# Kernel optimization log

Hardware: AMD Instinct MI355X
Metric: run time of the kernel (lower is better)

The kernel has to match this reference:

```python
import jax, jax.numpy as jnp
import numpy as np

N, E = 50000, 800000
DIN, DH, DOUT = 128, 128, 64


def setup_inputs() -> dict:
    key = jax.random.key(0)
    ks = jax.random.split(key, 18)
    s = 0.05
    inp = {
        "x": jax.random.normal(ks[0], (N, DIN), dtype=jnp.float32),
        "edge_index": jax.random.randint(ks[1], (2, E), 0, N, dtype=jnp.int64),
        # conv1 MLP: Linear(DIN,DH), Linear(DH,DH)
        "c1_w1": jax.random.normal(ks[2], (DIN, DH), dtype=jnp.float32) * s,
        "c1_b1": jax.random.normal(ks[3], (DH,), dtype=jnp.float32) * s,
        "c1_w2": jax.random.normal(ks[4], (DH, DH), dtype=jnp.float32) * s,
        "c1_b2": jax.random.normal(ks[5], (DH,), dtype=jnp.float32) * s,
        # conv2 MLP
        "c2_w1": jax.random.normal(ks[6], (DH, DH), dtype=jnp.float32) * s,
        "c2_b1": jax.random.normal(ks[7], (DH,), dtype=jnp.float32) * s,
        "c2_w2": jax.random.normal(ks[8], (DH, DH), dtype=jnp.float32) * s,
        "c2_b2": jax.random.normal(ks[9], (DH,), dtype=jnp.float32) * s,
        # conv3 MLP
        "c3_w1": jax.random.normal(ks[10], (DH, DH), dtype=jnp.float32) * s,
        "c3_b1": jax.random.normal(ks[11], (DH,), dtype=jnp.float32) * s,
        "c3_w2": jax.random.normal(ks[12], (DH, DH), dtype=jnp.float32) * s,
        "c3_b2": jax.random.normal(ks[13], (DH,), dtype=jnp.float32) * s,
        # output head
        "lin1_w": jax.random.normal(ks[14], (DH, DH), dtype=jnp.float32) * s,
        "lin1_b": jax.random.normal(ks[15], (DH,), dtype=jnp.float32) * s,
        "lin2_w": jax.random.normal(ks[16], (DH, DOUT), dtype=jnp.float32) * s,
        "lin2_b": jax.random.normal(ks[17], (DOUT,), dtype=jnp.float32) * s,
    }
    return inp


def _gin_conv(h, src, dst, w1, b1, w2, b2):
    # PyG GINConv, eps=0: MLP((1+eps)*x + sum_{j->i} x_j)
    agg = jax.ops.segment_sum(h[src], dst, num_segments=h.shape[0])  # [N, D]
    z = h + agg
    z = jax.nn.relu(z @ w1 + b1)
    return jax.nn.relu(z @ w2 + b2)


def reference(x, edge_index, c1_w1, c1_b1, c1_w2, c1_b2,
              c2_w1, c2_b1, c2_w2, c2_b2,
              c3_w1, c3_b1, c3_w2, c3_b2,
              lin1_w, lin1_b, lin2_w, lin2_b):
    src, dst = edge_index[0], edge_index[1]
    h = _gin_conv(x, src, dst, c1_w1, c1_b1, c1_w2, c1_b2)
    h = jax.nn.relu(h)  # redundant after MLP ReLU, but faithful to source
    h = _gin_conv(h, src, dst, c2_w1, c2_b1, c2_w2, c2_b2)
    h = jax.nn.relu(h)
    h = _gin_conv(h, src, dst, c3_w1, c3_b1, c3_w2, c3_b2)
    h = jax.nn.relu(h @ lin1_w + lin1_b)
    return h @ lin2_w + lin2_b  # [N, DOUT]
```

## Files before the change

### kernel.cpp

```cpp
#include <hip/hip_runtime.h>
#include <hip/hip_bf16.h>

typedef __attribute__((ext_vector_type(8))) short bf16x8;
typedef __attribute__((ext_vector_type(4))) float f32x4;

#define DH 128
#define DOUT 64

static __device__ __forceinline__ unsigned short f2bf(float f) {
    __hip_bfloat16 h = __float2bfloat16(f);
    return *(unsigned short*)&h;
}
static __device__ __forceinline__ void acc2(float& a0, float& a1, unsigned int u) {
    a0 += __uint_as_float(u << 16);
    a1 += __uint_as_float(u & 0xffff0000u);
}


struct WPrep {
    const float* src[8];
    unsigned short* dst[8];
};

__global__ void prep_kernel(const float* __restrict__ x, unsigned short* __restrict__ xb,
                            int n4, WPrep p, int* __restrict__ cnt, int N_) {
    int id = blockIdx.x * blockDim.x + threadIdx.x;
    if (id < n4) {
        float4 v = ((const float4*)x)[id];
        ushort4 b;
        b.x = f2bf(v.x); b.y = f2bf(v.y); b.z = f2bf(v.z); b.w = f2bf(v.w);
        ((ushort4*)xb)[id] = b;
        return;
    }
    id -= n4;
    if (id < N_) { cnt[id] = 0; return; }
    id -= N_;
    int m, off;
    if (id < 7 * 16384) { m = id >> 14; off = id & 16383; }
    else {
        m = 7; off = id - 7 * 16384;
        if (off >= 8192) return;
    }
    int shift = (m == 7) ? 6 : 7;
    int nc = 1 << shift;
    int k = off >> shift;
    int n = off & (nc - 1);
    p.dst[m][n * 128 + k] = f2bf(p.src[m][off]);
}


__global__ void hist_kernel(const int* __restrict__ dst, int* __restrict__ cnt,
                            int* __restrict__ rank, int E, int n) {
    int e = blockIdx.x * blockDim.x + threadIdx.x;
    if (e < E) {
        int d = dst[e];
        if ((unsigned)d < (unsigned)n) rank[e] = atomicAdd(&cnt[d], 1);
    }
}

__global__ void scan1_kernel(const int* __restrict__ cnt, int* __restrict__ rp_part,
                             int* __restrict__ bsum, int n) {
    __shared__ int s[256];
    int tid = threadIdx.x;
    int i = blockIdx.x * 256 + tid;
    int v = (i < n) ? cnt[i] : 0;
    s[tid] = v;
    __syncthreads();
    for (int off = 1; off < 256; off <<= 1) {
        int t = (tid >= off) ? s[tid - off] : 0;
        __syncthreads();
        s[tid] += t;
        __syncthreads();
    }
    if (i < n) rp_part[i] = s[tid] - v;
    if (tid == 255) bsum[blockIdx.x] = s[255];
}

__global__ void scan2_kernel(int* __restrict__ bsum, int nb) {
    __shared__ int s[256];
    int tid = threadIdx.x;
    int v = (tid < nb) ? bsum[tid] : 0;
    s[tid] = v;
    __syncthreads();
    for (int off = 1; off < 256; off <<= 1) {
        int t = (tid >= off) ? s[tid - off] : 0;
        __syncthreads();
        s[tid] += t;
        __syncthreads();
    }
    if (tid < nb) bsum[tid] = s[tid] - v;
}

__global__ void scan3_fill_kernel(const int* __restrict__ rp_part, const int* __restrict__ bsum,
                                  int* __restrict__ row_ptr,
                                  const int* __restrict__ src, const int* __restrict__ dst,
                                  const int* __restrict__ rank, int* __restrict__ esrc,
                                  int n, int E) {
    int gid = blockIdx.x * blockDim.x + threadIdx.x;
    if (gid < n) row_ptr[gid] = rp_part[gid] + bsum[gid >> 8];
    else if (gid == n) row_ptr[n] = E;
    if (gid < E) {
        int d = dst[gid];
        if ((unsigned)d < (unsigned)n)
            esrc[rp_part[d] + bsum[d >> 8] + rank[gid]] = src[gid];
    }
}


template <bool HEAD>
__launch_bounds__(256, 6)
__global__ void layer_kernel(const unsigned short* __restrict__ h,
                             const int* __restrict__ row_ptr,
                             const int* __restrict__ esrc,
                             const unsigned short* __restrict__ W1t,
                             const float* __restrict__ b1,
                             const unsigned short* __restrict__ W2t,
                             const float* __restrict__ b2,
                             const unsigned short* __restrict__ W3t,
                             const float* __restrict__ b3,
                             const unsigned short* __restrict__ W4t,
                             const float* __restrict__ b4,
                             void* __restrict__ outp, int M) {
    constexpr int LDA = 128 + 8;
    __shared__ __align__(16) unsigned short As[16][LDA];
    __shared__ __align__(16) unsigned short Zs[16][LDA];

    int tid = threadIdx.x;
    int wave = __builtin_amdgcn_readfirstlane(tid >> 6);
    int lane = tid & 63;
    int grp = lane >> 4;
    int c = lane & 15;
    int row0 = blockIdx.x * 16;
    int nodes0 = row0 + wave * 4;

    int b[4], e[4];
#pragma unroll
    for (int i = 0; i < 4; ++i) {
        int nd = nodes0 + i;
        b[i] = (nd < M) ? row_ptr[nd] : 0;
        e[i] = (nd < M) ? row_ptr[nd + 1] : 0;
    }
    float acc[4][8];
#pragma unroll
    for (int i = 0; i < 4; ++i)
#pragma unroll
        for (int j = 0; j < 8; ++j) acc[i][j] = 0.f;

    int pos[4];
#pragma unroll
    for (int i = 0; i < 4; ++i) pos[i] = b[i] + grp;
    int itmax = 0;
#pragma unroll
    for (int i = 0; i < 4; ++i) {
        int it = (e[i] - b[i] + 3) >> 2;
        itmax = it > itmax ? it : itmax;
    }

    for (int it = 0; it < itmax; ++it) {
        int idx[4] = {0, 0, 0, 0};
#pragma unroll
        for (int i = 0; i < 4; ++i)
            if (pos[i] < e[i]) idx[i] = esrc[pos[i]];
        uint4 u[4];
#pragma unroll
        for (int i = 0; i < 4; ++i) u[i] = make_uint4(0u, 0u, 0u, 0u);
#pragma unroll
        for (int i = 0; i < 4; ++i)
            if (pos[i] < e[i])
                u[i] = *((const uint4*)((const char*)h + ((size_t)idx[i] << 8)) + c);
#pragma unroll
        for (int i = 0; i < 4; ++i) {
            acc2(acc[i][0], acc[i][1], u[i].x);
            acc2(acc[i][2], acc[i][3], u[i].y);
            acc2(acc[i][4], acc[i][5], u[i].z);
            acc2(acc[i][6], acc[i][7], u[i].w);
            pos[i] += 4;
        }
    }

#pragma unroll
    for (int i = 0; i < 4; ++i) {
        int nd = nodes0 + i;
#pragma unroll
        for (int j = 0; j < 8; ++j) {
            float v = acc[i][j];
            v += __shfl_xor(v, 16, 64);
            v += __shfl_xor(v, 32, 64);
            acc[i][j] = v;
        }
        if (nd < M) {
            uint4 s = *((const uint4*)((const char*)h + ((size_t)nd << 8)) + c);
            acc2(acc[i][0], acc[i][1], s.x);
            acc2(acc[i][2], acc[i][3], s.y);
            acc2(acc[i][4], acc[i][5], s.z);
            acc2(acc[i][6], acc[i][7], s.w);
        }
        if (grp == 0) {
            uint4 ov;
            ov.x = (unsigned)f2bf(acc[i][0]) | ((unsigned)f2bf(acc[i][1]) << 16);
            ov.y = (unsigned)f2bf(acc[i][2]) | ((unsigned)f2bf(acc[i][3]) << 16);
            ov.z = (unsigned)f2bf(acc[i][4]) | ((unsigned)f2bf(acc[i][5]) << 16);
            ov.w = (unsigned)f2bf(acc[i][6]) | ((unsigned)f2bf(acc[i][7]) << 16);
            *(uint4*)(&As[wave * 4 + i][c * 8]) = ov;
        }
    }
    __syncthreads();

    int quad = lane >> 4;
    int l16 = lane & 15;

    bf16x8 af[4];
#pragma unroll
    for (int kt = 0; kt < 4; ++kt)
        af[kt] = *(const bf16x8*)(&As[l16][kt * 32 + quad * 8]);
#pragma unroll
    for (int p = 0; p < 2; ++p) {
        int ncol = (wave * 2 + p) * 16 + l16;
        const unsigned short* wp = W1t + ncol * 128 + quad * 8;
        f32x4 a = {0.f, 0.f, 0.f, 0.f};
#pragma unroll
        for (int kt = 0; kt < 4; ++kt)
            a = __builtin_amdgcn_mfma_f32_16x16x32_bf16(
                af[kt], *(const bf16x8*)(wp + kt * 32), a, 0, 0, 0);
        float bs = b1[ncol];
#pragma unroll
        for (int r = 0; r < 4; ++r) {
            float v = a[r] + bs;
            if (v < 0.f) v = 0.f;
            Zs[quad * 4 + r][ncol] = f2bf(v);
        }
    }
    __syncthreads();

    bf16x8 zf[4];
#pragma unroll
    for (int kt = 0; kt < 4; ++kt)
        zf[kt] = *(const bf16x8*)(&Zs[l16][kt * 32 + quad * 8]);
#pragma unroll
    for (int p = 0; p < 2; ++p) {
        int ncol = (wave * 2 + p) * 16 + l16;
        const unsigned short* wp = W2t + ncol * 128 + quad * 8;
        f32x4 a = {0.f, 0.f, 0.f, 0.f};
#pragma unroll
        for (int kt = 0; kt < 4; ++kt)
            a = __builtin_amdgcn_mfma_f32_16x16x32_bf16(
                zf[kt], *(const bf16x8*)(wp + kt * 32), a, 0, 0, 0);
        float bs = b2[ncol];
#pragma unroll
        for (int r = 0; r < 4; ++r) {
            float v = a[r] + bs;
            if (v < 0.f) v = 0.f;
            if (HEAD) {
                As[quad * 4 + r][ncol] = f2bf(v);
            } else {
                int grow = row0 + quad * 4 + r;
                if (grow < M)
                    ((unsigned short*)outp)[(size_t)grow * 128 + ncol] = f2bf(v);
            }
        }
    }

    if (HEAD) {
        __syncthreads();
        bf16x8 hf[4];
#pragma unroll
        for (int kt = 0; kt < 4; ++kt)
            hf[kt] = *(const bf16x8*)(&As[l16][kt * 32 + quad * 8]);
#pragma unroll
        for (int p = 0; p < 2; ++p) {
            int ncol = (wave * 2 + p) * 16 + l16;
            const unsigned short* wp = W3t + ncol * 128 + quad * 8;
            f32x4 a = {0.f, 0.f, 0.f, 0.f};
#pragma unroll
            for (int kt = 0; kt < 4; ++kt)
                a = __builtin_amdgcn_mfma_f32_16x16x32_bf16(
                    hf[kt], *(const bf16x8*)(wp + kt * 32), a, 0, 0, 0);
            float bs = b3[ncol];
#pragma unroll
            for (int r = 0; r < 4; ++r) {
                float v = a[r] + bs;
                if (v < 0.f) v = 0.f;
                Zs[quad * 4 + r][ncol] = f2bf(v);
            }
        }
        __syncthreads();
        bf16x8 gf[4];
#pragma unroll
        for (int kt = 0; kt < 4; ++kt)
            gf[kt] = *(const bf16x8*)(&Zs[l16][kt * 32 + quad * 8]);
        {
            int ncol = wave * 16 + l16;
            const unsigned short* wp = W4t + ncol * 128 + quad * 8;
            f32x4 a = {0.f, 0.f, 0.f, 0.f};
#pragma unroll
            for (int kt = 0; kt < 4; ++kt)
                a = __builtin_amdgcn_mfma_f32_16x16x32_bf16(
                    gf[kt], *(const bf16x8*)(wp + kt * 32), a, 0, 0, 0);
            float bs = b4[ncol];
#pragma unroll
            for (int r = 0; r < 4; ++r) {
                int grow = row0 + quad * 4 + r;
                if (grow < M)
                    ((float*)outp)[(size_t)grow * 64 + ncol] = a[r] + bs;
            }
        }
    }
}


extern "C" void kernel_launch(void* const* d_in, const int* in_sizes, int n_in,
                              void* d_out, int out_size, void* d_ws, size_t ws_size,
                              hipStream_t stream) {
    const float* x = (const float*)d_in[0];
    const int* ei = (const int*)d_in[1];
    int N = in_sizes[0] / DH;
    int E = in_sizes[1] / 2;
    const int* src = ei;
    const int* dstv = ei + E;

    char* ws = (char*)d_ws;
    size_t off = 0;
    auto alloc = [&](size_t bytes) -> void* {
        void* p = ws + off;
        off += (bytes + 255) & ~(size_t)255;
        return p;
    };
    unsigned short* xb = (unsigned short*)alloc((size_t)N * DH * 2);
    unsigned short* hA = (unsigned short*)alloc((size_t)N * DH * 2);
    unsigned short* hB = (unsigned short*)alloc((size_t)N * DH * 2);
    unsigned short* wt[8];
    for (int m = 0; m < 8; ++m) wt[m] = (unsigned short*)alloc(16384 * 2);
    int* cnt     = (int*)alloc((size_t)N * 4);
    int* rp_part = (int*)alloc((size_t)N * 4);
    int* row_ptr = (int*)alloc((size_t)(N + 1) * 4);
    int* rank    = (int*)alloc((size_t)E * 4);
    int* bsum    = (int*)alloc(256 * 4);
    int* esrc    = (int*)alloc((size_t)E * 4);

    WPrep wp;
    wp.src[0] = (const float*)d_in[2];
    wp.src[1] = (const float*)d_in[4];
    wp.src[2] = (const float*)d_in[6];
    wp.src[3] = (const float*)d_in[8];
    wp.src[4] = (const float*)d_in[10];
    wp.src[5] = (const float*)d_in[12];
    wp.src[6] = (const float*)d_in[14];
    wp.src[7] = (const float*)d_in[16];
    for (int m = 0; m < 8; ++m) wp.dst[m] = wt[m];
    int n4 = N * DH / 4;
    int prep_items = n4 + N + 7 * 16384 + 8192;
    prep_kernel<<<(prep_items + 255) / 256, 256, 0, stream>>>(x, xb, n4, wp, cnt, N);

    int nb = (N + 255) / 256;
    int eb = (E + 255) / 256;
    hist_kernel<<<eb, 256, 0, stream>>>(dstv, cnt, rank, E, N);
    scan1_kernel<<<nb, 256, 0, stream>>>(cnt, rp_part, bsum, N);
    scan2_kernel<<<1, 256, 0, stream>>>(bsum, nb);
    scan3_fill_kernel<<<eb, 256, 0, stream>>>(rp_part, bsum, row_ptr,
                                              src, dstv, rank, esrc, N, E);

    int gb = (N + 15) / 16;

    const float* c1b1 = (const float*)d_in[3];
    const float* c1b2 = (const float*)d_in[5];
    const float* c2b1 = (const float*)d_in[7];
    const float* c2b2 = (const float*)d_in[9];
    const float* c3b1 = (const float*)d_in[11];
    const float* c3b2 = (const float*)d_in[13];
    const float* l1b  = (const float*)d_in[15];
    const float* l2b  = (const float*)d_in[17];

    layer_kernel<false><<<gb, 256, 0, stream>>>(
        xb, row_ptr, esrc, wt[0], c1b1, wt[1], c1b2,
        nullptr, nullptr, nullptr, nullptr, hA, N);
    layer_kernel<false><<<gb, 256, 0, stream>>>(
        hA, row_ptr, esrc, wt[2], c2b1, wt[3], c2b2,
        nullptr, nullptr, nullptr, nullptr, hB, N);
    layer_kernel<true><<<gb, 256, 0, stream>>>(
        hB, row_ptr, esrc, wt[4], c3b1, wt[5], c3b2,
        wt[6], l1b, wt[7], l2b, d_out, N);
}
```

Measured before the change: 364.2 us.

## Pad CSR rows to multiples of 16 with a zero dummy node for branchless gathers

Each node's neighbour count is rounded up to a multiple of 16 in the scan. The padded slots of the edge list point at an extra all-zero row N appended to each feature buffer. The aggregation loop then drops per-edge bounds checks and issues 8 independent row gathers per half-iteration. The self-feature load moves to the start, and launch bounds drop from 6 to 4 blocks per unit to leave room for more registers. The cost is extra gathers of the cached dummy row, a larger esrc buffer that the prep kernel must fill, and unguarded reads if N is not a multiple of 16.

```diff
diff --git a/kernel.cpp b/kernel.cpp
--- a/kernel.cpp
+++ b/kernel.cpp
@@ -14,6 +14,12 @@
 static __device__ __forceinline__ void acc2(float& a0, float& a1, unsigned int u) {
     a0 += __uint_as_float(u << 16);
     a1 += __uint_as_float(u & 0xffff0000u);
+}
+static __device__ __forceinline__ void accq(float* a, const uint4& u) {
+    acc2(a[0], a[1], u.x);
+    acc2(a[2], a[3], u.y);
+    acc2(a[4], a[5], u.z);
+    acc2(a[6], a[7], u.w);
 }
 
 
@@ -23,7 +29,9 @@
 };
 
 __global__ void prep_kernel(const float* __restrict__ x, unsigned short* __restrict__ xb,
-                            int n4, WPrep p, int* __restrict__ cnt, int N_) {
+                            unsigned short* __restrict__ hA, unsigned short* __restrict__ hB,
+                            int n4, WPrep p, int* __restrict__ cnt,
+                            int* __restrict__ esrc, int Epad, int N_) {
     int id = blockIdx.x * blockDim.x + threadIdx.x;
     if (id < n4) {
         float4 v = ((const float4*)x)[id];
@@ -35,17 +43,27 @@
     id -= n4;
     if (id < N_) { cnt[id] = 0; return; }
     id -= N_;
-    int m, off;
-    if (id < 7 * 16384) { m = id >> 14; off = id & 16383; }
-    else {
-        m = 7; off = id - 7 * 16384;
-        if (off >= 8192) return;
-    }
-    int shift = (m == 7) ? 6 : 7;
-    int nc = 1 << shift;
-    int k = off >> shift;
-    int n = off & (nc - 1);
-    p.dst[m][n * 128 + k] = f2bf(p.src[m][off]);
+    if (id < 7 * 16384 + 8192) {
+        int m, off;
+        if (id < 7 * 16384) { m = id >> 14; off = id & 16383; }
+        else { m = 7; off = id - 7 * 16384; }
+        int shift = (m == 7) ? 6 : 7;
+        int nc = 1 << shift;
+        int k = off >> shift;
+        int n = off & (nc - 1);
+        p.dst[m][n * 128 + k] = f2bf(p.src[m][off]);
+        return;
+    }
+    id -= 7 * 16384 + 8192;
+    if (id < 3 * 128) {
+        int j = id & 127, w = id >> 7;
+        if (w == 0) xb[(size_t)N_ * 128 + j] = 0;
+        else if (w == 1) hA[(size_t)N_ * 128 + j] = 0;
+        else hB[(size_t)N_ * 128 + j] = 0;
+        return;
+    }
+    id -= 384;
+    if (id < Epad) esrc[id] = N_;
 }
 
 
@@ -63,7 +81,7 @@
     __shared__ int s[256];
     int tid = threadIdx.x;
     int i = blockIdx.x * 256 + tid;
-    int v = (i < n) ? cnt[i] : 0;
+    int v = (i < n) ? ((cnt[i] + 15) & ~15) : 0;
     s[tid] = v;
     __syncthreads();
     for (int off = 1; off < 256; off <<= 1) {
@@ -72,7 +90,7 @@
         s[tid] += t;
         __syncthreads();
     }
-    if (i < n) rp_part[i] = s[tid] - v;
+    if (i <= n) rp_part[i] = s[tid] - v;
     if (tid == 255) bsum[blockIdx.x] = s[255];
 }
 
@@ -97,8 +115,7 @@
                                   const int* __restrict__ rank, int* __restrict__ esrc,
                                   int n, int E) {
     int gid = blockIdx.x * blockDim.x + threadIdx.x;
-    if (gid < n) row_ptr[gid] = rp_part[gid] + bsum[gid >> 8];
-    else if (gid == n) row_ptr[n] = E;
+    if (gid <= n) row_ptr[gid] = rp_part[gid] + bsum[gid >> 8];
     if (gid < E) {
         int d = dst[gid];
         if ((unsigned)d < (unsigned)n)
@@ -108,9 +125,9 @@
 
 
 template <bool HEAD>
-__launch_bounds__(256, 6)
+__launch_bounds__(256, 4)
 __global__ void layer_kernel(const unsigned short* __restrict__ h,
-                             const int* __restrict__ row_ptr,
+                             const int* __restrict__ rp,
                              const int* __restrict__ esrc,
                              const unsigned short* __restrict__ W1t,
                              const float* __restrict__ b1,
@@ -131,69 +148,64 @@
     int grp = lane >> 4;
     int c = lane & 15;
     int row0 = blockIdx.x * 16;
-    int nodes0 = row0 + wave * 4;
-
-    int b[4], e[4];
+    int nd0 = row0 + wave * 4;
+
+    const uint4* hq = (const uint4*)h;
+
+    uint4 s[4];
+#pragma unroll
+    for (int i = 0; i < 4; ++i) s[i] = hq[(nd0 + i) * 16 + c];
+
+    int b[4], rn[4];
 #pragma unroll
     for (int i = 0; i < 4; ++i) {
-        int nd = nodes0 + i;
-        b[i] = (nd < M) ? row_ptr[nd] : 0;
-        e[i] = (nd < M) ? row_ptr[nd + 1] : 0;
-    }
+        int rb = rp[nd0 + i], re = rp[nd0 + i + 1];
+        b[i] = rb;
+        rn[i] = (re - rb) >> 4;
+    }
+
     float acc[4][8];
 #pragma unroll
     for (int i = 0; i < 4; ++i)
 #pragma unroll
         for (int j = 0; j < 8; ++j) acc[i][j] = 0.f;
 
-    int pos[4];
-#pragma unroll
-    for (int i = 0; i < 4; ++i) pos[i] = b[i] + grp;
-    int itmax = 0;
+    if (grp == 0) {
+#pragma unroll
+        for (int i = 0; i < 4; ++i) accq(acc[i], s[i]);
+    }
+
+    int maxr = max(max(rn[0], rn[1]), max(rn[2], rn[3]));
+    for (int r = 0; r < maxr; ++r) {
+#pragma unroll
+        for (int half = 0; half < 2; ++half) {
+            int idx[8];
+#pragma unroll
+            for (int t = 0; t < 8; ++t) {
+                int i = half * 2 + (t >> 2);
+                idx[t] = esrc[b[i] + (r << 4) + ((t & 3) << 2) + grp];
+            }
+#pragma unroll
+            for (int t = 0; t < 8; ++t) {
+                int i = half * 2 + (t >> 2);
+                idx[t] = (r < rn[i]) ? idx[t] : M;
+            }
+            uint4 u[8];
+#pragma unroll
+            for (int t = 0; t < 8; ++t) u[t] = hq[idx[t] * 16 + c];
+#pragma unroll
+            for (int t = 0; t < 8; ++t) accq(acc[half * 2 + (t >> 2)], u[t]);
+        }
+    }
+
 #pragma unroll
     for (int i = 0; i < 4; ++i) {
-        int it = (e[i] - b[i] + 3) >> 2;
-        itmax = it > itmax ? it : itmax;
-    }
-
-    for (int it = 0; it < itmax; ++it) {
-        int idx[4] = {0, 0, 0, 0};
-#pragma unroll
-        for (int i = 0; i < 4; ++i)
-            if (pos[i] < e[i]) idx[i] = esrc[pos[i]];
-        uint4 u[4];
-#pragma unroll
-        for (int i = 0; i < 4; ++i) u[i] = make_uint4(0u, 0u, 0u, 0u);
-#pragma unroll
-        for (int i = 0; i < 4; ++i)
-            if (pos[i] < e[i])
-                u[i] = *((const uint4*)((const char*)h + ((size_t)idx[i] << 8)) + c);
-#pragma unroll
-        for (int i = 0; i < 4; ++i) {
-            acc2(acc[i][0], acc[i][1], u[i].x);
-            acc2(acc[i][2], acc[i][3], u[i].y);
-            acc2(acc[i][4], acc[i][5], u[i].z);
-            acc2(acc[i][6], acc[i][7], u[i].w);
-            pos[i] += 4;
-        }
-    }
-
-#pragma unroll
-    for (int i = 0; i < 4; ++i) {
-        int nd = nodes0 + i;
 #pragma unroll
         for (int j = 0; j < 8; ++j) {
             float v = acc[i][j];
             v += __shfl_xor(v, 16, 64);
             v += __shfl_xor(v, 32, 64);
             acc[i][j] = v;
-        }
-        if (nd < M) {
-            uint4 s = *((const uint4*)((const char*)h + ((size_t)nd << 8)) + c);
-            acc2(acc[i][0], acc[i][1], s.x);
-            acc2(acc[i][2], acc[i][3], s.y);
-            acc2(acc[i][4], acc[i][5], s.z);
-            acc2(acc[i][6], acc[i][7], s.w);
         }
         if (grp == 0) {
             uint4 ov;
@@ -317,6 +329,7 @@
     int E = in_sizes[1] / 2;
     const int* src = ei;
     const int* dstv = ei + E;
+    int Epad = E + 15 * N + 1024;
 
     char* ws = (char*)d_ws;
     size_t off = 0;
@@ -325,17 +338,17 @@
         off += (bytes + 255) & ~(size_t)255;
         return p;
     };
-    unsigned short* xb = (unsigned short*)alloc((size_t)N * DH * 2);
-    unsigned short* hA = (unsigned short*)alloc((size_t)N * DH * 2);
-    unsigned short* hB = (unsigned short*)alloc((size_t)N * DH * 2);
+    unsigned short* xb = (unsigned short*)alloc((size_t)(N + 1) * DH * 2);
+    unsigned short* hA = (unsigned short*)alloc((size_t)(N + 1) * DH * 2);
+    unsigned short* hB = (unsigned short*)alloc((size_t)(N + 1) * DH * 2);
     unsigned short* wt[8];
     for (int m = 0; m < 8; ++m) wt[m] = (unsigned short*)alloc(16384 * 2);
     int* cnt     = (int*)alloc((size_t)N * 4);
-    int* rp_part = (int*)alloc((size_t)N * 4);
+    int* rp_part = (int*)alloc((size_t)(N + 1) * 4);
     int* row_ptr = (int*)alloc((size_t)(N + 1) * 4);
     int* rank    = (int*)alloc((size_t)E * 4);
     int* bsum    = (int*)alloc(256 * 4);
-    int* esrc    = (int*)alloc((size_t)E * 4);
+    int* esrc    = (int*)alloc((size_t)Epad * 4);
 
     WPrep wp;
     wp.src[0] = (const float*)d_in[2];
@@ -348,10 +361,11 @@
     wp.src[7] = (const float*)d_in[16];
     for (int m = 0; m < 8; ++m) wp.dst[m] = wt[m];
     int n4 = N * DH / 4;
-    int prep_items = n4 + N + 7 * 16384 + 8192;
-    prep_kernel<<<(prep_items + 255) / 256, 256, 0, stream>>>(x, xb, n4, wp, cnt, N);
-
-    int nb = (N + 255) / 256;
+    int prep_items = n4 + N + 7 * 16384 + 8192 + 384 + Epad;
+    prep_kernel<<<(prep_items + 255) / 256, 256, 0, stream>>>(
+        x, xb, hA, hB, n4, wp, cnt, esrc, Epad, N);
+
+    int nb = (N + 1 + 255) / 256;
     int eb = (E + 255) / 256;
     hist_kernel<<<eb, 256, 0, stream>>>(dstv, cnt, rank, E, N);
     scan1_kernel<<<nb, 256, 0, stream>>>(cnt, rp_part, bsum, N);
```

New measurement: 350.7 us. -3.7%, faster.
